# Optimization experiments

Hardware: AMD Instinct MI355X
Metric: run time of the kernel (lower is better)

Reference implementation:

```python
import jax, jax.numpy as jnp
import numpy as np

B, T, E, V, L = 8, 128, 256, 8192, 5  # batch, block_size, embedding_size (== num heads, head_size=1), vocab, num blocks


def setup_inputs() -> dict:
    key = jax.random.key(0)
    ks = jax.random.split(key, 12)
    s = 0.02
    return {
        "idxs": jax.random.randint(ks[0], (B, T), 0, V),
        "targets": jax.random.randint(ks[1], (B, T), 0, V),
        "emb": jax.random.normal(ks[2], (V, E)) * s,
        "pos_emb": jax.random.normal(ks[3], (T, E)) * s,
        "Wq": jax.random.normal(ks[4], (L, E, E)) * s,  # per-layer: E heads, each Linear(E,1); columns are heads
        "Wk": jax.random.normal(ks[5], (L, E, E)) * s,
        "Wv": jax.random.normal(ks[6], (L, E, E)) * s,
        "Wfc": jax.random.normal(ks[7], (L, E, E)) * s,
        "bfc": jnp.zeros((L, E)),
        "Wlm": jax.random.normal(ks[8], (E, V)) * s,
        "blm": jnp.zeros((V,)),
    }


def _block(x, Wq, Wk, Wv, Wfc, bfc):
    # E heads of head_size=1: projecting with [E,E] gives [B,T,H] with H==E,
    # column h being head h's scalar q/k/v. Faithful to per-head Linear(E,1).
    q = x @ Wq
    k = x @ Wk
    v = x @ Wv
    scores = jnp.einsum('bih,bjh->bhij', q, k)  # no 1/sqrt(d) scaling (faithful)
    i = jnp.arange(x.shape[1])
    causal = i[:, None] >= i[None, :]  # masked_fill where tril==0, i.e. j>i -> -inf
    scores = jnp.where(causal[None, None], scores, -jnp.inf)
    attn = jax.nn.softmax(scores, axis=-2)  # NOTE: source softmaxes over dim=-2 (query axis) -- faithful quirk
    out = jnp.einsum('bhij,bjh->bih', attn, v)  # concat of heads == H axis order
    x = x + out
    return x + jax.nn.relu(x @ Wfc + bfc)


def reference(idxs, targets, emb, pos_emb, Wq, Wk, Wv, Wfc, bfc, Wlm, blm):
    x = emb[idxs] + pos_emb[: idxs.shape[1]]  # [B,T,E]
    for l in range(L):
        x = _block(x, Wq[l], Wk[l], Wv[l], Wfc[l], bfc[l])
    logits = (x @ Wlm + blm).reshape(-1, V)  # [B*T, V], as source views before CE
    logp = jax.nn.log_softmax(logits, axis=-1)
    loss = -jnp.take_along_axis(logp, targets.reshape(-1, 1), axis=-1).mean()
    return logits, loss
```

## Files before the change

### kernel.cpp

```cpp
#include <hip/hip_runtime.h>

#define BB 8
#define TT 128
#define EE 256
#define VV 8192
#define LL 5
#define NROWS (BB*TT)

typedef __attribute__((ext_vector_type(8))) short bf16x8;
typedef __attribute__((ext_vector_type(4))) float f32x4;

__device__ inline ushort f2bf(float f) {
    union { float f; unsigned u; } c; c.f = f;
    unsigned u = c.u;
    return (ushort)((u + 0x7FFF + ((u >> 16) & 1)) >> 16);
}

__device__ __forceinline__ void gload_lds16(const void* g, void* l) {
    __builtin_amdgcn_global_load_lds((const __attribute__((address_space(1))) unsigned int*)g,
                                     (__attribute__((address_space(3))) unsigned int*)l,
                                     16, 0, 0);
}


__global__ __launch_bounds__(512, 2) void layer0_kernel(
        const int* __restrict__ idxs, const float* __restrict__ emb, const float* __restrict__ pos,
        const float* __restrict__ Wq, const float* __restrict__ Wk,
        const float* __restrict__ Wv, const float* __restrict__ Wfc,
        const float* __restrict__ Wlm,
        float* __restrict__ y_out, ushort* __restrict__ WTs, ushort* __restrict__ WlmT,
        float* __restrict__ loss_cell) {
    __shared__ __align__(16) ushort Xs[128*128];
    __shared__ __align__(16) ushort Bs[32*128];
    __shared__ __align__(16) float QS[8*132], KS[8*132], VS[8*132], MS[8*132], RV[8*132];
    int tid = threadIdx.x, lane = tid & 63, w = tid >> 6;
    int blk = blockIdx.x;

    if (blk >= 256) {
        int id = blk - 256;
        if (id == 0) {
            if (tid == 0) *loss_cell = 0.f;
            return;
        }
        ushort (*ts)[72] = (ushort(*)[72])Xs;
        if (id < 513) {
            int idw = id - 1;
            int v0 = (idw & 127) * 64, k0 = (idw >> 7) * 64;
            for (int kk = w; kk < 64; kk += 8)
                ts[lane][kk] = f2bf(Wlm[(size_t)(k0 + kk)*VV + v0 + lane]);
            __syncthreads();
            for (int vv = w; vv < 64; vv += 8) {
                int r = v0 + vv, k = k0 + lane;
                WlmT[(size_t)r*256 + (k & 128) + ((k & 127) ^ ((r & 7) << 3))] = ts[vv][lane];
            }
            return;
        }
        {
            int idm = id - 513;
            int mat = idm >> 4, tile = idm & 15;
            int l = mat >> 2, type = mat & 3;
            const float* src = (type == 0 ? Wq : type == 1 ? Wk : type == 2 ? Wv : Wfc) + l*EE*EE;
            ushort* dst = WTs + mat*EE*EE;
            int i0 = (tile >> 2) * 64, o0 = (tile & 3) * 64;
            for (int ii = w; ii < 64; ii += 8)
                ts[lane][ii] = f2bf(src[(i0 + ii)*EE + o0 + lane]);
            __syncthreads();
            for (int oo = w; oo < 64; oo += 8) {
                int r = o0 + oo, k = i0 + lane;
                dst[(size_t)r*256 + (k & 128) + ((k & 127) ^ ((r & 7) << 3))] = ts[oo][lane];
            }
            return;
        }
    }

    int b  = blk >> 5;
    int h0 = (blk & 31) * 8;

    f32x4 acc[2] = {};
    int rband = w*16 + (lane & 15);
    int kq = (lane >> 4) * 8;

    #pragma unroll
    for (int half = 0; half < 2; ++half) {
        if (half) __syncthreads();
        {
            int rsub = lane >> 5, cb = (lane & 31) * 4;
            for (int rr2 = w*2; rr2 < 128; rr2 += 16) {
                int rr = rr2 + rsub;
                int id = idxs[b*TT + rr];
                float4 v = *(const float4*)&emb[(size_t)id*EE + half*128 + cb];
                float4 p = *(const float4*)&pos[rr*EE + half*128 + cb];
                ushort4 hh;
                hh.x = f2bf(v.x + p.x); hh.y = f2bf(v.y + p.y);
                hh.z = f2bf(v.z + p.z); hh.w = f2bf(v.w + p.w);
                *(ushort4*)&Xs[rr*128 + (cb ^ ((rr & 7) << 3))] = hh;
            }
        }
        {
            int c = tid >> 4;
            int kb8 = (tid & 15) * 8;
            ushort tmp[8];
            if (c < 24) {
                int mat = c >> 3;
                int col = h0 + (c & 7);
                const float* Wm = mat == 0 ? Wq : (mat == 1 ? Wk : Wv);
                #pragma unroll
                for (int i = 0; i < 8; ++i)
                    tmp[i] = f2bf(Wm[(size_t)(half*128 + kb8 + i)*EE + col]);
            } else {
                #pragma unroll
                for (int i = 0; i < 8; ++i) tmp[i] = 0;
            }
            ushort* dst = &Bs[c*128 + (kb8 ^ ((c & 7) << 3))];
            *(ushort4*)dst       = *(ushort4*)&tmp[0];
            *(ushort4*)(dst + 4) = *(ushort4*)&tmp[4];
        }
        __syncthreads();
        for (int ks = 0; ks < 4; ++ks) {
            int kk = ks*32 + kq;
            bf16x8 a = *(const bf16x8*)&Xs[rband*128 + (kk ^ ((rband & 7) << 3))];
            #pragma unroll
            for (int ct = 0; ct < 2; ++ct) {
                int c = ct*16 + (lane & 15);
                bf16x8 bb = *(const bf16x8*)&Bs[c*128 + (kk ^ ((c & 7) << 3))];
                acc[ct] = __builtin_amdgcn_mfma_f32_16x16x32_bf16(a, bb, acc[ct], 0, 0, 0);
            }
        }
    }
    {
        int r_ = w*16 + ((lane >> 4) << 2);
        #pragma unroll
        for (int ct = 0; ct < 2; ++ct) {
            int col24 = ct*16 + (lane & 15);
            #pragma unroll
            for (int j = 0; j < 4; ++j) {
                float val = acc[ct][j];
                int row = r_ + j;
                if (col24 < 8)       QS[col24*132 + row] = val;
                else if (col24 < 16) KS[(col24-8)*132 + row] = val;
                else if (col24 < 24) VS[(col24-16)*132 + row] = val;
            }
        }
    }
    __syncthreads();

    int g = w, lg = lane;
    {
        int j0 = lg*2;
        float k0 = KS[g*132 + j0], k1 = KS[g*132 + j0 + 1];
        float q0j = QS[g*132 + j0], q1j = QS[g*132 + j0 + 1];
        float pmax = fmaxf(q0j, q1j), pmin = fminf(q0j, q1j);
        #pragma unroll
        for (int d = 1; d < 64; d <<= 1) {
            float om = __shfl_down(pmax, d);
            float on = __shfl_down(pmin, d);
            if (lg + d < 64) { pmax = fmaxf(pmax, om); pmin = fminf(pmin, on); }
        }
        float nx = __shfl_down(pmax, 1), nn = __shfl_down(pmin, 1);
        float sp1 = (lg == 63) ? q1j : fmaxf(q1j, nx);
        float sn1 = (lg == 63) ? q1j : fminf(q1j, nn);
        float m0 = (k0 >= 0.f) ? k0*pmax : k0*pmin;
        float m1 = (k1 >= 0.f) ? k1*sp1  : k1*sn1;
        float z0 = 0.f, z1 = 0.f;
        for (int i = j0; i < TT; ++i) {
            float qi = QS[g*132 + i];
            z0 += __expf(qi*k0 - m0);
            z1 += (i >= j0+1) ? __expf(qi*k1 - m1) : 0.f;
        }
        MS[g*132 + j0]     = m0;
        MS[g*132 + j0 + 1] = m1;
        RV[g*132 + j0]     = VS[g*132 + j0] / z0;
        RV[g*132 + j0 + 1] = VS[g*132 + j0 + 1] / z1;
    }
    __syncthreads();
    float a0 = 0.f, a1 = 0.f;
    {
        int i0 = lg*2;
        float q0 = QS[g*132 + i0], q1 = QS[g*132 + i0 + 1];
        for (int j = 0; j <= i0 + 1; ++j) {
            float kj = KS[g*132 + j], mj = MS[g*132 + j], rj = RV[g*132 + j];
            float e0 = __expf(q0*kj - mj) * rj;
            float e1 = __expf(q1*kj - mj) * rj;
            a0 += (j <= i0) ? e0 : 0.f;
            a1 += e1;
        }
    }
    __syncthreads();
    VS[g*132 + lg*2]     = a0;
    VS[g*132 + lg*2 + 1] = a1;
    __syncthreads();

    {
        int row = tid >> 2, cp = (tid & 3) * 2;
        int id = idxs[b*TT + row];
        float2 ev = *(const float2*)&emb[(size_t)id*EE + h0 + cp];
        float2 pv = *(const float2*)&pos[row*EE + h0 + cp];
        float2 ov;
        ov.x = ev.x + pv.x + VS[cp*132 + row];
        ov.y = ev.y + pv.y + VS[(cp+1)*132 + row];
        *(float2*)&y_out[(size_t)(b*TT + row)*EE + h0 + cp] = ov;
    }
}

__global__ __launch_bounds__(512, 4) void qkv_attn_kernel(
        float* __restrict__ x, const ushort* __restrict__ WTl) {
    __shared__ __align__(16) ushort Xs[128*128];
    __shared__ __align__(16) ushort Bs[32*128];
    __shared__ __align__(16) float QS[8*132], KS[8*132], VS[8*132], MS[8*132], RV[8*132];
    int tid = threadIdx.x, lane = tid & 63, w = tid >> 6;
    int b  = blockIdx.x >> 5;
    int h0 = (blockIdx.x & 31) * 8;

    f32x4 acc[2] = {};
    int rband = w*16 + (lane & 15);
    int kq = (lane >> 4) * 8;

    #pragma unroll
    for (int half = 0; half < 2; ++half) {
        if (half) __syncthreads();
        {
            int rsub = lane >> 5, cb = (lane & 31) * 4;
            for (int rr2 = w*2; rr2 < 128; rr2 += 16) {
                int rr = rr2 + rsub;
                float4 v = *(const float4*)&x[(size_t)(b*TT + rr)*EE + half*128 + cb];
                ushort4 hh; hh.x = f2bf(v.x); hh.y = f2bf(v.y); hh.z = f2bf(v.z); hh.w = f2bf(v.w);
                *(ushort4*)&Xs[rr*128 + (cb ^ ((rr & 7) << 3))] = hh;
            }
        }
        {
            int rowg = w*4 + (lane >> 4);
            int rowv = rowg < 24 ? rowg : 23;
            int mat = rowv >> 3, col = h0 + (rowv & 7);
            const ushort* src = WTl + (size_t)mat*EE*EE + (size_t)col*256
                              + half*128 + (lane & 15)*8;
            gload_lds16(src, &Bs[(size_t)w*4*128]);
        }
        __syncthreads();
        for (int ks = 0; ks < 4; ++ks) {
            int kk = ks*32 + kq;
            bf16x8 a = *(const bf16x8*)&Xs[rband*128 + (kk ^ ((rband & 7) << 3))];
            #pragma unroll
            for (int ct = 0; ct < 2; ++ct) {
                int c = ct*16 + (lane & 15);
                bf16x8 bb = *(const bf16x8*)&Bs[c*128 + (kk ^ ((c & 7) << 3))];
                acc[ct] = __builtin_amdgcn_mfma_f32_16x16x32_bf16(a, bb, acc[ct], 0, 0, 0);
            }
        }
    }
    {
        int r_ = w*16 + ((lane >> 4) << 2);
        #pragma unroll
        for (int ct = 0; ct < 2; ++ct) {
            int col24 = ct*16 + (lane & 15);
            #pragma unroll
            for (int j = 0; j < 4; ++j) {
                float val = acc[ct][j];
                int row = r_ + j;
                if (col24 < 8)       QS[col24*132 + row] = val;
                else if (col24 < 16) KS[(col24-8)*132 + row] = val;
                else if (col24 < 24) VS[(col24-16)*132 + row] = val;
            }
        }
    }
    __syncthreads();

    int g = w, lg = lane;
    {
        int j0 = lg*2;
        float k0 = KS[g*132 + j0], k1 = KS[g*132 + j0 + 1];
        float q0j = QS[g*132 + j0], q1j = QS[g*132 + j0 + 1];
        float pmax = fmaxf(q0j, q1j), pmin = fminf(q0j, q1j);
        #pragma unroll
        for (int d = 1; d < 64; d <<= 1) {
            float om = __shfl_down(pmax, d);
            float on = __shfl_down(pmin, d);
            if (lg + d < 64) { pmax = fmaxf(pmax, om); pmin = fminf(pmin, on); }
        }
        float nx = __shfl_down(pmax, 1), nn = __shfl_down(pmin, 1);
        float sp1 = (lg == 63) ? q1j : fmaxf(q1j, nx);
        float sn1 = (lg == 63) ? q1j : fminf(q1j, nn);
        float m0 = (k0 >= 0.f) ? k0*pmax : k0*pmin;
        float m1 = (k1 >= 0.f) ? k1*sp1  : k1*sn1;
        float z0 = 0.f, z1 = 0.f;
        for (int i = j0; i < TT; ++i) {
            float qi = QS[g*132 + i];
            z0 += __expf(qi*k0 - m0);
            z1 += (i >= j0+1) ? __expf(qi*k1 - m1) : 0.f;
        }
        MS[g*132 + j0]     = m0;
        MS[g*132 + j0 + 1] = m1;
        RV[g*132 + j0]     = VS[g*132 + j0] / z0;
        RV[g*132 + j0 + 1] = VS[g*132 + j0 + 1] / z1;
    }
    __syncthreads();
    float a0 = 0.f, a1 = 0.f;
    {
        int i0 = lg*2;
        float q0 = QS[g*132 + i0], q1 = QS[g*132 + i0 + 1];
        for (int j = 0; j <= i0 + 1; ++j) {
            float kj = KS[g*132 + j], mj = MS[g*132 + j], rj = RV[g*132 + j];
            float e0 = __expf(q0*kj - mj) * rj;
            float e1 = __expf(q1*kj - mj) * rj;
            a0 += (j <= i0) ? e0 : 0.f;
            a1 += e1;
        }
    }
    __syncthreads();
    VS[g*132 + lg*2]     = a0;
    VS[g*132 + lg*2 + 1] = a1;
    __syncthreads();

    {
        int row = tid >> 2, cp = (tid & 3) * 2;
        size_t gx = (size_t)(b*TT + row)*EE + h0 + cp;
        float2 xv = *(float2*)&x[gx];
        xv.x += VS[cp*132 + row];
        xv.y += VS[(cp+1)*132 + row];
        *(float2*)&x[gx] = xv;
    }
}

__global__ __launch_bounds__(256, 4) void fc_mfma(
        const float* __restrict__ xin, const ushort* __restrict__ WT,
        const float* __restrict__ bfc, float* __restrict__ xout) {
    __shared__ __align__(16) ushort As[64*128];
    __shared__ __align__(16) ushort Bs[64*128];
    int tid = threadIdx.x, lane = tid & 63, w = tid >> 6;
    int c0 = blockIdx.x * 64;
    int r0 = blockIdx.y * 64;

    f32x4 acc[4] = {};
    int rband = w*16 + (lane & 15);
    int kq = (lane >> 4) * 8;

    #pragma unroll
    for (int half = 0; half < 2; ++half) {
        if (half) __syncthreads();
        {
            int rsub = lane >> 5, cb = (lane & 31) * 4;
            for (int rr2 = w*2; rr2 < 64; rr2 += 8) {
                int rr = rr2 + rsub;
                float4 v = *(const float4*)&xin[(size_t)(r0 + rr)*EE + half*128 + cb];
                ushort4 hh; hh.x = f2bf(v.x); hh.y = f2bf(v.y); hh.z = f2bf(v.z); hh.w = f2bf(v.w);
                *(ushort4*)&As[rr*128 + (cb ^ ((rr & 7) << 3))] = hh;
            }
        }
        for (int rg = w*4; rg < 64; rg += 16) {
            int row = c0 + rg + (lane >> 4);
            const ushort* src = WT + (size_t)row*256 + half*128 + (lane & 15)*8;
            gload_lds16(src, &Bs[(size_t)rg*128]);
        }
        __syncthreads();
        for (int ks = 0; ks < 4; ++ks) {
            int kk = ks*32 + kq;
            bf16x8 a = *(const bf16x8*)&As[rband*128 + (kk ^ ((rband & 7) << 3))];
            #pragma unroll
            for (int n = 0; n < 4; ++n) {
                int c = n*16 + (lane & 15);
                bf16x8 b = *(const bf16x8*)&Bs[c*128 + (kk ^ ((c & 7) << 3))];
                acc[n] = __builtin_amdgcn_mfma_f32_16x16x32_bf16(a, b, acc[n], 0, 0, 0);
            }
        }
    }
    int grow0 = r0 + w*16 + ((lane >> 4) << 2);
    #pragma unroll
    for (int n = 0; n < 4; ++n) {
        int col = c0 + n*16 + (lane & 15);
        float bias = bfc[col];
        #pragma unroll
        for (int j = 0; j < 4; ++j) {
            size_t idx = (size_t)(grow0 + j)*EE + col;
            xout[idx] = xin[idx] + fmaxf(acc[n][j] + bias, 0.f);
        }
    }
}

__global__ __launch_bounds__(512, 4) void lm_mfma_kernel(
        const float* __restrict__ x, const ushort* __restrict__ WlmT,
        const float* __restrict__ blm, float* __restrict__ out,
        float* __restrict__ pm, float* __restrict__ pz) {
    __shared__ __align__(16) char LDSb[128*132*4];
    ushort* As = (ushort*)LDSb;
    ushort* Bs = (ushort*)LDSb + 128*128;
    float*  fst = (float*)LDSb;
    int tid = threadIdx.x;
    int lane = tid & 63, w = tid >> 6;
    int c0 = blockIdx.x * 128;
    int r0 = blockIdx.y * 128;

    int wr = (w >> 2) * 64, wc = (w & 3) * 32;
    f32x4 acc[4][2] = {};
    int kq = (lane >> 4) * 8;

    #pragma unroll
    for (int half = 0; half < 2; ++half) {
        if (half) __syncthreads();
        {
            int rsub = lane >> 5, cb = (lane & 31) * 4;
            for (int rr2 = w*2; rr2 < 128; rr2 += 16) {
                int rr = rr2 + rsub;
                float4 v = *(const float4*)&x[(size_t)(r0 + rr)*EE + half*128 + cb];
                ushort4 hh; hh.x = f2bf(v.x); hh.y = f2bf(v.y); hh.z = f2bf(v.z); hh.w = f2bf(v.w);
                *(ushort4*)&As[rr*128 + (cb ^ ((rr & 7) << 3))] = hh;
            }
        }
        for (int rg = w*4; rg < 128; rg += 32) {
            int row = c0 + rg + (lane >> 4);
            const ushort* src = WlmT + (size_t)row*256 + half*128 + (lane & 15)*8;
            gload_lds16(src, &Bs[(size_t)rg*128]);
        }
        __syncthreads();
        for (int ks = 0; ks < 4; ++ks) {
            int kk = ks*32 + kq;
            bf16x8 a[4], bfr[2];
            #pragma unroll
            for (int m = 0; m < 4; ++m) {
                int rband = wr + m*16 + (lane & 15);
                a[m] = *(const bf16x8*)&As[rband*128 + (kk ^ ((rband & 7) << 3))];
            }
            #pragma unroll
            for (int n = 0; n < 2; ++n) {
                int c = wc + n*16 + (lane & 15);
                bfr[n] = *(const bf16x8*)&Bs[c*128 + (kk ^ ((c & 7) << 3))];
            }
            #pragma unroll
            for (int m = 0; m < 4; ++m)
                #pragma unroll
                for (int n = 0; n < 2; ++n)
                    acc[m][n] = __builtin_amdgcn_mfma_f32_16x16x32_bf16(a[m], bfr[n], acc[m][n], 0, 0, 0);
        }
    }
    __syncthreads();

    float bias[2];
    #pragma unroll
    for (int n = 0; n < 2; ++n) bias[n] = blm[c0 + wc + n*16 + (lane & 15)];
    #pragma unroll
    for (int m = 0; m < 4; ++m) {
        int rw = wr + m*16 + (lane >> 4)*4;
        #pragma unroll
        for (int j = 0; j < 4; ++j) {
            int row = rw + j;
            float vals[2];
            float vmax = -INFINITY;
            #pragma unroll
            for (int n = 0; n < 2; ++n) {
                vals[n] = acc[m][n][j] + bias[n];
                fst[row*132 + wc + n*16 + (lane & 15)] = vals[n];
                vmax = fmaxf(vmax, vals[n]);
            }
            #pragma unroll
            for (int msk = 1; msk <= 8; msk <<= 1) vmax = fmaxf(vmax, __shfl_xor(vmax, msk));
            float z = 0.f;
            #pragma unroll
            for (int n = 0; n < 2; ++n) z += __expf(vals[n] - vmax);
            #pragma unroll
            for (int msk = 1; msk <= 8; msk <<= 1) z += __shfl_xor(z, msk);
            if ((lane & 15) == 0) {
                pm[(size_t)(r0 + row)*256 + blockIdx.x*4 + (w & 3)] = vmax;
                pz[(size_t)(r0 + row)*256 + blockIdx.x*4 + (w & 3)] = z;
            }
        }
    }
    __syncthreads();
    #pragma unroll
    for (int it = 0; it < 8; ++it) {
        int k = tid + it*512;
        int row = k >> 5, c4 = (k & 31)*4;
        float4 v = *(float4*)&fst[row*132 + c4];
        *(float4*)&out[(size_t)(r0 + row)*VV + c0 + c4] = v;
    }
}

__global__ void loss_kernel(const float* __restrict__ pm, const float* __restrict__ pz,
                            const float* __restrict__ logits, const int* __restrict__ targets,
                            float* __restrict__ out_last) {
    int r = blockIdx.x;
    int t = threadIdx.x;
    __shared__ float sm[256], sz[256];
    float m = pm[(size_t)r*256 + t];
    float z = pz[(size_t)r*256 + t];
    sm[t] = m; __syncthreads();
    for (int s = 128; s > 0; s >>= 1) {
        if (t < s) sm[t] = fmaxf(sm[t], sm[t + s]);
        __syncthreads();
    }
    float M = sm[0];
    sz[t] = z * __expf(m - M); __syncthreads();
    for (int s = 128; s > 0; s >>= 1) {
        if (t < s) sz[t] += sz[t + s];
        __syncthreads();
    }
    if (t == 0) {
        float lse = M + logf(sz[0]);
        atomicAdd(out_last, (lse - logits[(size_t)r*VV + targets[r]]) * (1.0f / NROWS));
    }
}

extern "C" void kernel_launch(void* const* d_in, const int* in_sizes, int n_in,
                              void* d_out, int out_size, void* d_ws, size_t ws_size,
                              hipStream_t stream) {
    const int*   idxs    = (const int*)d_in[0];
    const int*   targets = (const int*)d_in[1];
    const float* emb     = (const float*)d_in[2];
    const float* pos     = (const float*)d_in[3];
    const float* Wq      = (const float*)d_in[4];
    const float* Wk      = (const float*)d_in[5];
    const float* Wv      = (const float*)d_in[6];
    const float* Wfc     = (const float*)d_in[7];
    const float* bfc     = (const float*)d_in[8];
    const float* Wlm     = (const float*)d_in[9];
    const float* blm     = (const float*)d_in[10];
    float* out = (float*)d_out;
    float* loss_cell = out + (size_t)NROWS * VV;

    float* ws = (float*)d_ws;
    float*  ya   = ws;
    float*  yb   = ya + NROWS*EE;
    float*  pm   = yb + NROWS*EE;
    float*  pz   = pm + NROWS*256;
    ushort* WTs  = (ushort*)(pz + NROWS*256);
    ushort* WlmT = WTs + 20*EE*EE;

    layer0_kernel<<<1089, 512, 0, stream>>>(idxs, emb, pos, Wq, Wk, Wv, Wfc, Wlm,
                                            ya, WTs, WlmT, loss_cell);
    fc_mfma<<<dim3(4, 16), 256, 0, stream>>>(ya, WTs + (size_t)3*EE*EE, bfc, yb);

    for (int l = 1; l < LL; ++l) {
        float* xi = (l & 1) ? yb : ya;
        float* xo = (l & 1) ? ya : yb;
        qkv_attn_kernel<<<256, 512, 0, stream>>>(xi, WTs + (size_t)l*4*EE*EE);
        fc_mfma<<<dim3(4, 16), 256, 0, stream>>>(xi, WTs + (size_t)(l*4 + 3)*EE*EE,
                                                 bfc + (size_t)l*EE, xo);
    }

    lm_mfma_kernel<<<dim3(VV/128, NROWS/128), 512, 0, stream>>>(yb, WlmT, blm, out, pm, pz);
    loss_kernel<<<NROWS, 256, 0, stream>>>(pm, pz, out, targets, loss_cell);
}
```

Before: 202.4 us.

## Compute attention exponentials once and reuse them for both normalizer and output

Restructures the per-head softmax-over-queries attention so each exp(q_i*k_j - m_j) is computed once. Each lane holds a 32-row by one-column tile, reduces the column normalizer with cross-lane shuffles, and accumulates the weighted outputs in registers, then reduces across lanes. This replaces the old two-pass scheme that evaluated the exponentials twice with a barrier in between, and removes the RV shared buffer. In exchange it computes the full 128x128 tile including masked entries instead of exploiting causal skipping, and it raises register pressure with the 64-float arrays.

```diff
diff --git a/kernel.cpp b/kernel.cpp
--- a/kernel.cpp
+++ b/kernel.cpp
@@ -32,7 +32,7 @@
         float* __restrict__ loss_cell) {
     __shared__ __align__(16) ushort Xs[128*128];
     __shared__ __align__(16) ushort Bs[32*128];
-    __shared__ __align__(16) float QS[8*132], KS[8*132], VS[8*132], MS[8*132], RV[8*132];
+    __shared__ __align__(16) float QS[8*132], KS[8*132], VS[8*132], MS[8*132];
     int tid = threadIdx.x, lane = tid & 63, w = tid >> 6;
     int blk = blockIdx.x;
 
@@ -159,35 +159,54 @@
         float nx = __shfl_down(pmax, 1), nn = __shfl_down(pmin, 1);
         float sp1 = (lg == 63) ? q1j : fmaxf(q1j, nx);
         float sn1 = (lg == 63) ? q1j : fminf(q1j, nn);
-        float m0 = (k0 >= 0.f) ? k0*pmax : k0*pmin;
-        float m1 = (k1 >= 0.f) ? k1*sp1  : k1*sn1;
-        float z0 = 0.f, z1 = 0.f;
-        for (int i = j0; i < TT; ++i) {
-            float qi = QS[g*132 + i];
-            z0 += __expf(qi*k0 - m0);
-            z1 += (i >= j0+1) ? __expf(qi*k1 - m1) : 0.f;
-        }
-        MS[g*132 + j0]     = m0;
-        MS[g*132 + j0 + 1] = m1;
-        RV[g*132 + j0]     = VS[g*132 + j0] / z0;
-        RV[g*132 + j0 + 1] = VS[g*132 + j0 + 1] / z1;
-    }
-    __syncthreads();
-    float a0 = 0.f, a1 = 0.f;
-    {
-        int i0 = lg*2;
-        float q0 = QS[g*132 + i0], q1 = QS[g*132 + i0 + 1];
-        for (int j = 0; j <= i0 + 1; ++j) {
-            float kj = KS[g*132 + j], mj = MS[g*132 + j], rj = RV[g*132 + j];
-            float e0 = __expf(q0*kj - mj) * rj;
-            float e1 = __expf(q1*kj - mj) * rj;
-            a0 += (j <= i0) ? e0 : 0.f;
-            a1 += e1;
-        }
-    }
-    __syncthreads();
-    VS[g*132 + lg*2]     = a0;
-    VS[g*132 + lg*2 + 1] = a1;
+        MS[g*132 + j0]     = (k0 >= 0.f) ? k0*pmax : k0*pmin;
+        MS[g*132 + j0 + 1] = (k1 >= 0.f) ? k1*sp1  : k1*sn1;
+    }
+    __syncthreads();
+
+    {
+        float outp[32];
+        #pragma unroll
+        for (int r = 0; r < 32; ++r) outp[r] = 0.f;
+        int c = lg & 15, rg = lg >> 4;
+        int rbase = rg * 32;
+        for (int jt = 0; jt < 8; ++jt) {
+            int j = jt*16 + c;
+            float kj = KS[g*132 + j];
+            float mj = MS[g*132 + j];
+            float vj = VS[g*132 + j];
+            float P[32];
+            float z = 0.f;
+            #pragma unroll
+            for (int r = 0; r < 32; ++r) {
+                int i = rbase + r;
+                float e = __expf(QS[g*132 + i] * kj - mj);
+                e = (i >= j) ? e : 0.f;
+                P[r] = e;
+                z += e;
+            }
+            z += __shfl_xor(z, 16);
+            z += __shfl_xor(z, 32);
+            float rv = vj / z;
+            #pragma unroll
+            for (int r = 0; r < 32; ++r) outp[r] += P[r] * rv;
+        }
+        #pragma unroll
+        for (int r = 0; r < 32; ++r) {
+            float v = outp[r];
+            v += __shfl_xor(v, 1);
+            v += __shfl_xor(v, 2);
+            v += __shfl_xor(v, 4);
+            v += __shfl_xor(v, 8);
+            outp[r] = v;
+        }
+        __syncthreads();
+        if (c == 0) {
+            #pragma unroll
+            for (int r = 0; r < 32; ++r)
+                VS[g*132 + rbase + r] = outp[r];
+        }
+    }
     __syncthreads();
 
     {
@@ -206,7 +225,7 @@
         float* __restrict__ x, const ushort* __restrict__ WTl) {
     __shared__ __align__(16) ushort Xs[128*128];
     __shared__ __align__(16) ushort Bs[32*128];
-    __shared__ __align__(16) float QS[8*132], KS[8*132], VS[8*132], MS[8*132], RV[8*132];
+    __shared__ __align__(16) float QS[8*132], KS[8*132], VS[8*132], MS[8*132];
     int tid = threadIdx.x, lane = tid & 63, w = tid >> 6;
     int b  = blockIdx.x >> 5;
     int h0 = (blockIdx.x & 31) * 8;
@@ -279,35 +298,54 @@
         float nx = __shfl_down(pmax, 1), nn = __shfl_down(pmin, 1);
         float sp1 = (lg == 63) ? q1j : fmaxf(q1j, nx);
         float sn1 = (lg == 63) ? q1j : fminf(q1j, nn);
-        float m0 = (k0 >= 0.f) ? k0*pmax : k0*pmin;
-        float m1 = (k1 >= 0.f) ? k1*sp1  : k1*sn1;
-        float z0 = 0.f, z1 = 0.f;
-        for (int i = j0; i < TT; ++i) {
-            float qi = QS[g*132 + i];
-            z0 += __expf(qi*k0 - m0);
-            z1 += (i >= j0+1) ? __expf(qi*k1 - m1) : 0.f;
-        }
-        MS[g*132 + j0]     = m0;
-        MS[g*132 + j0 + 1] = m1;
-        RV[g*132 + j0]     = VS[g*132 + j0] / z0;
-        RV[g*132 + j0 + 1] = VS[g*132 + j0 + 1] / z1;
-    }
-    __syncthreads();
-    float a0 = 0.f, a1 = 0.f;
-    {
-        int i0 = lg*2;
-        float q0 = QS[g*132 + i0], q1 = QS[g*132 + i0 + 1];
-        for (int j = 0; j <= i0 + 1; ++j) {
-            float kj = KS[g*132 + j], mj = MS[g*132 + j], rj = RV[g*132 + j];
-            float e0 = __expf(q0*kj - mj) * rj;
-            float e1 = __expf(q1*kj - mj) * rj;
-            a0 += (j <= i0) ? e0 : 0.f;
-            a1 += e1;
-        }
-    }
-    __syncthreads();
-    VS[g*132 + lg*2]     = a0;
-    VS[g*132 + lg*2 + 1] = a1;
+        MS[g*132 + j0]     = (k0 >= 0.f) ? k0*pmax : k0*pmin;
+        MS[g*132 + j0 + 1] = (k1 >= 0.f) ? k1*sp1  : k1*sn1;
+    }
+    __syncthreads();
+
+    {
+        float outp[32];
+        #pragma unroll
+        for (int r = 0; r < 32; ++r) outp[r] = 0.f;
+        int c = lg & 15, rg = lg >> 4;
+        int rbase = rg * 32;
+        for (int jt = 0; jt < 8; ++jt) {
+            int j = jt*16 + c;
+            float kj = KS[g*132 + j];
+            float mj = MS[g*132 + j];
+            float vj = VS[g*132 + j];
+            float P[32];
+            float z = 0.f;
+            #pragma unroll
+            for (int r = 0; r < 32; ++r) {
+                int i = rbase + r;
+                float e = __expf(QS[g*132 + i] * kj - mj);
+                e = (i >= j) ? e : 0.f;
+                P[r] = e;
+                z += e;
+            }
+            z += __shfl_xor(z, 16);
+            z += __shfl_xor(z, 32);
+            float rv = vj / z;
+            #pragma unroll
+            for (int r = 0; r < 32; ++r) outp[r] += P[r] * rv;
+        }
+        #pragma unroll
+        for (int r = 0; r < 32; ++r) {
+            float v = outp[r];
+            v += __shfl_xor(v, 1);
+            v += __shfl_xor(v, 2);
+            v += __shfl_xor(v, 4);
+            v += __shfl_xor(v, 8);
+            outp[r] = v;
+        }
+        __syncthreads();
+        if (c == 0) {
+            #pragma unroll
+            for (int r = 0; r < 32; ++r)
+                VS[g*132 + rbase + r] = outp[r];
+        }
+    }
     __syncthreads();
 
     {
```

New measurement: 203.5 us. Within noise of the previous version (+0.5%).
